# Performance work log

Measured on AMD Instinct MI355X. Metric: run time of the kernel, lower is better.

The kernel has to match this reference:

```python
import jax, jax.numpy as jnp
import numpy as np

EPS = 2.220446049250313e-16  # sys.float_info.epsilon, as in repo's feature_normalize
H_BW = 0.1  # bandwidth h (forward default)


def _feature_normalize(f):
    # L2 normalize over channel dim (dim=1) of [B, C, H, W]
    norm = jnp.sqrt(jnp.sum(f * f, axis=1, keepdims=True)) + EPS
    return f / norm


def setup_inputs() -> dict:
    key = jax.random.key(0)
    k1, k2 = jax.random.split(key)
    shape = (4, 256, 64, 64)
    return {
        "X_features": jax.random.normal(k1, shape, dtype=jnp.float32),
        "Y_features": jax.random.normal(k2, shape, dtype=jnp.float32),
    }


def reference(X_features, Y_features):
    B, C = X_features.shape[0], X_features.shape[1]
    # feature centering (opt.PONO = False branch): subtract Y's per-channel spatial mean
    y_mean = jnp.mean(Y_features.reshape(B, C, -1), axis=-1)[:, :, None, None]
    Xc = X_features - y_mean
    Yc = Y_features - y_mean
    # channel-wise L2 normalize, then flatten spatial dims -> [B, C, N]
    Xn = _feature_normalize(Xc).reshape(B, C, -1)
    Yn = _feature_normalize(Yc).reshape(B, C, -1)
    # pairwise cosine distance d: [B, N, N]
    d = 1.0 - jnp.einsum("bcn,bcm->bnm", Xn, Yn)
    # relative distance normalization by row-min
    d_min = jnp.min(d, axis=-1, keepdims=True)
    d_norm = d / (d_min + 0.001)
    # softmax-like contextual similarity weights
    w = jnp.exp((1.0 - d_norm) / H_BW)
    A_ij = w / jnp.sum(w, axis=-1, keepdims=True)
    # per-sample contextual similarity and loss
    CX = jnp.mean(jnp.max(A_ij, axis=-1), axis=1)  # [B]
    loss = -jnp.log(CX)
    return loss
```

## Files before the change

kernel.cpp:

```cpp
#include <hip/hip_runtime.h>
#include <hip/hip_bf16.h>
#include <stdint.h>


#define Bn 4
#define Cn 256
#define Nn 4096

typedef float  f32x16 __attribute__((ext_vector_type(16)));
typedef __bf16 bf16x8 __attribute__((ext_vector_type(8)));

#define GLD16(gp, lp) __builtin_amdgcn_global_load_lds(                      \
    (const __attribute__((address_space(1))) void*)(gp),                     \
    (__attribute__((address_space(3))) void*)(lp), 16, 0, 0)

#define LDbf(base, off) (*(const bf16x8*)((base) + (off)))
#define MFMA32(a, b, c) __builtin_amdgcn_mfma_f32_32x32x16_bf16((a), (b), (c), 0, 0, 0)

__global__ __launch_bounds__(256) void k_mean(const float* __restrict__ Y,
                                              float* __restrict__ ymean) {
  const int bc = blockIdx.x;
  const float4* p4 = (const float4*)(Y + (size_t)bc * 4096);
  float s = 0.f;
  #pragma unroll
  for (int i = 0; i < 4; ++i) {
    float4 v = p4[threadIdx.x + i * 256];
    s += (v.x + v.y) + (v.z + v.w);
  }
  #pragma unroll
  for (int m = 1; m < 64; m <<= 1) s += __shfl_xor(s, m);
  __shared__ float part[4];
  if ((threadIdx.x & 63) == 0) part[threadIdx.x >> 6] = s;
  __syncthreads();
  if (threadIdx.x == 0)
    ymean[bc] = (part[0] + part[1] + part[2] + part[3]) * (1.0f / 4096.0f);
}

__global__ __launch_bounds__(256) void k_pack(const float* __restrict__ X,
                                              const float* __restrict__ Y,
                                              const float* __restrict__ ymean,
                                              __hip_bfloat16* __restrict__ Xp,
                                              __hip_bfloat16* __restrict__ Yp,
                                              float* __restrict__ invnx,
                                              float* __restrict__ invny) {
  const int n0 = blockIdx.x * 64, b = blockIdx.y;
  __shared__ float mu[256];
  __shared__ float tile[64][65];
  __shared__ float part[8][64];
  const int t  = threadIdx.x;
  const int tc = t >> 6, tn = t & 63;
  const int oc = t & 63, on = t >> 6;
  mu[t] = ymean[b * 256 + t];
  __syncthreads();
  float psx = 0.f, psy = 0.f;
  for (int cc = 0; cc < 4; ++cc) {
    #pragma unroll 4
    for (int i = 0; i < 16; ++i) {
      int cl = i * 4 + tc;
      float v = X[((size_t)b * 256 + cc * 64 + cl) * 4096 + n0 + tn] - mu[cc * 64 + cl];
      tile[cl][tn] = v;
      psx += v * v;
    }
    __syncthreads();
    #pragma unroll 4
    for (int i = 0; i < 16; ++i) {
      int nl = i * 4 + on;
      Xp[((size_t)b * 4096 + n0 + nl) * 256 + cc * 64 + oc] = __float2bfloat16(tile[oc][nl]);
    }
    __syncthreads();
    #pragma unroll 4
    for (int i = 0; i < 16; ++i) {
      int cl = i * 4 + tc;
      float v = Y[((size_t)b * 256 + cc * 64 + cl) * 4096 + n0 + tn] - mu[cc * 64 + cl];
      tile[cl][tn] = v;
      psy += v * v;
    }
    __syncthreads();
    #pragma unroll 4
    for (int i = 0; i < 16; ++i) {
      int nl = i * 4 + on;
      Yp[((size_t)b * 4096 + n0 + nl) * 256 + cc * 64 + oc] = __float2bfloat16(tile[oc][nl]);
    }
    __syncthreads();
  }
  part[tc][tn] = psx;
  part[4 + tc][tn] = psy;
  __syncthreads();
  if (t < 64)
    invnx[b * 4096 + n0 + t] = rsqrtf(part[0][t] + part[1][t] + part[2][t] + part[3][t]);
  else if (t < 128) {
    int u = t - 64;
    invny[b * 4096 + n0 + u] = rsqrtf(part[4][u] + part[5][u] + part[6][u] + part[7][u]);
  }
}

template<int PASS>
__global__ __launch_bounds__(512, 1) void k_pass(const __hip_bfloat16* __restrict__ Xp,
                                                 const __hip_bfloat16* __restrict__ Yp,
                                                 const float* __restrict__ invnx,
                                                 const float* __restrict__ invny,
                                                 float* __restrict__ rmax_part,
                                                 float* __restrict__ ssum_part) {
  __shared__ __align__(16) char YsL[3][32768];
  __shared__ float invnyL[2048];
  __shared__ float redm[2][2][2][16][4];
  __shared__ float2 lammuL[128];

  const int tid = threadIdx.x;
  const int lane = tid & 63;
  const int w = tid >> 6;
  const int rg = w >> 2, cs = w & 3;
  const int l31 = lane & 31, hi = lane >> 5;
  const int hi16 = hi << 4;

  const int L = blockIdx.x;
  const int b = (L & 7) >> 1, half = L & 1;
  const int rowtile = L >> 3;
  const int rowg0 = b * Nn + rowtile * 128;
  const int colg0 = half * 2048;

  const char* Xgb = (const char*)Xp + (size_t)rowg0 * 512;
  const char* Yg  = (const char*)(Yp + ((size_t)b * Nn + colg0) * Cn);

  bf16x8 A[4][4][2];
  #pragma unroll
  for (int kp = 0; kp < 4; ++kp)
    #pragma unroll
    for (int s = 0; s < 4; ++s)
      #pragma unroll
      for (int ai = 0; ai < 2; ++ai)
        A[kp][s][ai] = *(const bf16x8*)(Xgb + (size_t)(rg * 64 + ai * 32 + l31) * 512
                                            + ((kp * 4 + s) * 32 + hi16));

  ((float4*)invnyL)[tid] = ((const float4*)(invny + b * Nn + colg0))[tid];
  if constexpr (PASS == 2) {
    if (tid < 128) {
      int rowg = rowg0 + tid;
      float mg = fmaxf(rmax_part[rowg], rmax_part[Bn * Nn + rowg]);
      float ix = invnx[rowg];
      float smax = mg * ix;
      float lam = (10.0f / (1.001f - smax)) * ix * 1.44269504f;
      lammuL[tid] = make_float2(lam, lam * mg);
    }
  }
  __syncthreads();

  int yoff[4];
  #pragma unroll
  for (int i = 0; i < 4; ++i) {
    int m = i * 64 + (tid >> 3);
    yoff[i] = m * 512 + (((tid & 7) * 16) ^ ((m & 7) << 4));
  }

#define STAGE_HALF(q, h)                                                      \
  { const int q_ = (q);                                                       \
    const char* src_ = Yg + (size_t)((q_ >> 2) * 131072 + (q_ & 3) * 128);    \
    char* dst_ = YsL[q_ % 3];                                                 \
    GLD16(src_ + yoff[2 * (h)],     dst_ + (2 * (h)) * 8192 + tid * 16);      \
    GLD16(src_ + yoff[2 * (h) + 1], dst_ + (2 * (h) + 1) * 8192 + tid * 16); }

  STAGE_HALF(0, 0); STAGE_HALF(0, 1);
  STAGE_HALF(1, 0); STAGE_HALF(1, 1);

  const int brow0 = cs * 64 + l31;
  const int bswz  = (brow0 & 7) << 4;

  f32x16 acc[2][2];
  #pragma unroll
  for (int ai = 0; ai < 2; ++ai)
    #pragma unroll
    for (int bj = 0; bj < 2; ++bj) acc[ai][bj] = (f32x16)0.0f;
  float accR[2][16];
  #pragma unroll
  for (int ai = 0; ai < 2; ++ai)
    #pragma unroll
    for (int r = 0; r < 16; ++r) accR[ai][r] = (PASS == 1) ? -3.0e38f : 0.f;

#define HARVEST()                                                             \
  { const int cb = mt * 256 + cs * 64 + l31;                                  \
    const float iny0 = invnyL[cb], iny1 = invnyL[cb + 32];                    \
    _Pragma("unroll")                                                         \
    for (int ai = 0; ai < 2; ++ai) {                                          \
      _Pragma("unroll")                                                       \
      for (int r = 0; r < 16; ++r) {                                          \
        if constexpr (PASS == 1) {                                            \
          accR[ai][r] = fmaxf(accR[ai][r],                                    \
              fmaxf(acc[ai][0][r] * iny0, acc[ai][1][r] * iny1));             \
        } else {                                                              \
          float2 lm = lammuL[rg * 64 + ai * 32 + (r & 3) + 8 * (r >> 2) + 4 * hi]; \
          accR[ai][r] += exp2f(fmaf(lm.x, acc[ai][0][r] * iny0, -lm.y))       \
                       + exp2f(fmaf(lm.x, acc[ai][1][r] * iny1, -lm.y));      \
        }                                                                     \
        acc[ai][0][r] = 0.f; acc[ai][1][r] = 0.f;                             \
      } } }

#define QUAD(KP, S, KB)                                                       \
  { bf16x8 b0_ = LDbf(yb_, brow0 * 128 + (((KB) + hi16) ^ bswz));             \
    bf16x8 b1_ = LDbf(yb_, (brow0 + 32) * 128 + (((KB) + hi16) ^ bswz));      \
    __builtin_amdgcn_s_setprio(1);                                            \
    acc[0][0] = MFMA32(A[KP][S][0], b0_, acc[0][0]);                          \
    acc[0][1] = MFMA32(A[KP][S][0], b1_, acc[0][1]);                          \
    acc[1][0] = MFMA32(A[KP][S][1], b0_, acc[1][0]);                          \
    acc[1][1] = MFMA32(A[KP][S][1], b1_, acc[1][1]);                          \
    __builtin_amdgcn_s_setprio(0); }

#define TILE(KP, WAITS, DO_STAGE)                                             \
  { const int p_ = mt * 4 + (KP);                                             \
    if (DO_STAGE) STAGE_HALF(p_ + 2, 0);                                      \
    asm volatile("s_waitcnt vmcnt(" WAITS ")" ::: "memory");                  \
    asm volatile("s_barrier" ::: "memory");                                   \
    const char* yb_ = YsL[p_ % 3];                                            \
    QUAD(KP, 0, 0)                                                            \
    QUAD(KP, 1, 32)                                                           \
    if (DO_STAGE) STAGE_HALF(p_ + 2, 1);                                      \
    QUAD(KP, 2, 64)                                                           \
    QUAD(KP, 3, 96)                                                           \
    if ((KP) == 3) HARVEST();                                                 \
    asm volatile("s_barrier" ::: "memory"); }

  for (int mt = 0; mt < 7; ++mt) {
    TILE(0, "6", true)
    TILE(1, "6", true)
    TILE(2, "6", true)
    TILE(3, "6", true)
  }
  {
    const int mt = 7;
    TILE(0, "6", true)
    TILE(1, "6", true)
    TILE(2, "4", false)
    TILE(3, "0", false)
  }
#undef TILE
#undef QUAD
#undef HARVEST
#undef STAGE_HALF

  #pragma unroll
  for (int ai = 0; ai < 2; ++ai)
    #pragma unroll
    for (int r = 0; r < 16; ++r) {
      float v = accR[ai][r];
      #pragma unroll
      for (int m = 1; m < 32; m <<= 1) {
        float o = __shfl_xor(v, m);
        v = (PASS == 1) ? fmaxf(v, o) : (v + o);
      }
      if (l31 == 0) redm[rg][hi][ai][r][cs] = v;
    }
  __syncthreads();
  if (tid < 128) {
    const int rgg = tid >> 6, rr = tid & 63;
    const int aii = (rr >> 5) & 1, r32 = rr & 31;
    const int hh = (r32 >> 2) & 1;
    const int reg = (r32 & 3) | (((r32 >> 3) & 3) << 2);
    float v0 = redm[rgg][hh][aii][reg][0], v1 = redm[rgg][hh][aii][reg][1];
    float v2 = redm[rgg][hh][aii][reg][2], v3 = redm[rgg][hh][aii][reg][3];
    if constexpr (PASS == 1)
      rmax_part[half * (Bn * Nn) + rowg0 + tid] = fmaxf(fmaxf(v0, v1), fmaxf(v2, v3));
    else
      ssum_part[half * (Bn * Nn) + rowg0 + tid] = v0 + v1 + v2 + v3;
  }
}

__global__ __launch_bounds__(256) void k_fin(const float* __restrict__ ssum_part,
                                             float* __restrict__ out) {
  const int b = blockIdx.x;
  float s = 0.f;
  #pragma unroll 4
  for (int i = 0; i < 16; ++i) {
    int row = b * Nn + threadIdx.x + i * 256;
    s += 1.0f / (ssum_part[row] + ssum_part[Bn * Nn + row]);
  }
  #pragma unroll
  for (int m = 1; m < 64; m <<= 1) s += __shfl_xor(s, m);
  __shared__ float part[4];
  if ((threadIdx.x & 63) == 0) part[threadIdx.x >> 6] = s;
  __syncthreads();
  if (threadIdx.x == 0)
    out[b] = -logf((part[0] + part[1] + part[2] + part[3]) * (1.0f / (float)Nn));
}

extern "C" void kernel_launch(void* const* d_in, const int* in_sizes, int n_in,
                              void* d_out, int out_size, void* d_ws, size_t ws_size,
                              hipStream_t stream) {
  const float* X = (const float*)d_in[0];
  const float* Y = (const float*)d_in[1];
  float* out = (float*)d_out;
  char* ws = (char*)d_ws;

  __hip_bfloat16* Xp = (__hip_bfloat16*)ws;
  __hip_bfloat16* Yp = (__hip_bfloat16*)(ws + 8388608);
  float* invnx = (float*)(ws + 16777216);
  float* invny = invnx + 16384;
  float* rmax  = invny + 16384;
  float* ssum  = rmax + 32768;
  float* ymean = ssum + 32768;

  k_mean  <<<Bn * Cn, 256, 0, stream>>>(Y, ymean);
  k_pack  <<<dim3(Nn / 64, Bn), 256, 0, stream>>>(X, Y, ymean, Xp, Yp, invnx, invny);
  k_pass<1><<<256, 512, 0, stream>>>(Xp, Yp, invnx, invny, rmax, ssum);
  k_pass<2><<<256, 512, 0, stream>>>(Xp, Yp, invnx, invny, rmax, ssum);
  k_fin   <<<Bn, 256, 0, stream>>>(ssum, out);
}
```

Baseline: 228.9 us.

## Move upper half of X operand from registers to swizzled LDS

Keeps only the first two K-slices of the X (A) operand in registers and stages the other half into a new 32 KB swizzled LDS buffer with async global-to-LDS loads. Tiles 2 and 3 of each column block now read A fragments from LDS alongside the B fragments. The kernel attribute changes from one block per CU to a 2-waves-per-EU hint, with the aim of cutting VGPR pressure and allowing more resident waves. In exchange it doubles LDS read traffic in half of the tiles and raises LDS use to roughly 137 KB, which likely still limits the CU to one 512-thread block.

```diff
diff --git a/kernel.cpp b/kernel.cpp
--- a/kernel.cpp
+++ b/kernel.cpp
@@ -95,13 +95,16 @@
 }
 
 template<int PASS>
-__global__ __launch_bounds__(512, 1) void k_pass(const __hip_bfloat16* __restrict__ Xp,
-                                                 const __hip_bfloat16* __restrict__ Yp,
-                                                 const float* __restrict__ invnx,
-                                                 const float* __restrict__ invny,
-                                                 float* __restrict__ rmax_part,
-                                                 float* __restrict__ ssum_part) {
+__global__ __launch_bounds__(512)
+__attribute__((amdgpu_waves_per_eu(2, 2)))
+void k_pass(const __hip_bfloat16* __restrict__ Xp,
+            const __hip_bfloat16* __restrict__ Yp,
+            const float* __restrict__ invnx,
+            const float* __restrict__ invny,
+            float* __restrict__ rmax_part,
+            float* __restrict__ ssum_part) {
   __shared__ __align__(16) char YsL[3][32768];
+  __shared__ __align__(16) char AsL[32768];
   __shared__ float invnyL[2048];
   __shared__ float redm[2][2][2][16][4];
   __shared__ float2 lammuL[128];
@@ -122,9 +125,9 @@
   const char* Xgb = (const char*)Xp + (size_t)rowg0 * 512;
   const char* Yg  = (const char*)(Yp + ((size_t)b * Nn + colg0) * Cn);
 
-  bf16x8 A[4][4][2];
-  #pragma unroll
-  for (int kp = 0; kp < 4; ++kp)
+  bf16x8 A[2][4][2];
+  #pragma unroll
+  for (int kp = 0; kp < 2; ++kp)
     #pragma unroll
     for (int s = 0; s < 4; ++s)
       #pragma unroll
@@ -145,6 +148,14 @@
   }
   __syncthreads();
 
+  #pragma unroll
+  for (int s = 0; s < 4; ++s) {
+    const int off = s * 8192 + tid * 16;
+    const int row = off >> 8;
+    const int col = off & 255;
+    GLD16(Xgb + (size_t)row * 512 + 256 + (col ^ ((row & 7) << 4)), AsL + off);
+  }
+
   int yoff[4];
   #pragma unroll
   for (int i = 0; i < 4; ++i) {
@@ -164,6 +175,8 @@
 
   const int brow0 = cs * 64 + l31;
   const int bswz  = (brow0 & 7) << 4;
+  const int arow0 = rg * 64 + l31;
+  const int aswz  = (l31 & 7) << 4;
 
   f32x16 acc[2][2];
   #pragma unroll
@@ -194,7 +207,7 @@
         acc[ai][0][r] = 0.f; acc[ai][1][r] = 0.f;                             \
       } } }
 
-#define QUAD(KP, S, KB)                                                       \
+#define QUAD_R(KP, S, KB)                                                     \
   { bf16x8 b0_ = LDbf(yb_, brow0 * 128 + (((KB) + hi16) ^ bswz));             \
     bf16x8 b1_ = LDbf(yb_, (brow0 + 32) * 128 + (((KB) + hi16) ^ bswz));      \
     __builtin_amdgcn_s_setprio(1);                                            \
@@ -204,35 +217,63 @@
     acc[1][1] = MFMA32(A[KP][S][1], b1_, acc[1][1]);                          \
     __builtin_amdgcn_s_setprio(0); }
 
-#define TILE(KP, WAITS, DO_STAGE)                                             \
-  { const int p_ = mt * 4 + (KP);                                             \
+#define QUAD_L(KP, S, KB)                                                     \
+  { const int ka_ = (((KP) - 2) * 4 + (S)) * 32 + hi16;                       \
+    bf16x8 a0_ = LDbf(AsL, arow0 * 256 + (ka_ ^ aswz));                       \
+    bf16x8 a1_ = LDbf(AsL, (arow0 + 32) * 256 + (ka_ ^ aswz));                \
+    bf16x8 b0_ = LDbf(yb_, brow0 * 128 + (((KB) + hi16) ^ bswz));             \
+    bf16x8 b1_ = LDbf(yb_, (brow0 + 32) * 128 + (((KB) + hi16) ^ bswz));      \
+    __builtin_amdgcn_s_setprio(1);                                            \
+    acc[0][0] = MFMA32(a0_, b0_, acc[0][0]);                                  \
+    acc[0][1] = MFMA32(a0_, b1_, acc[0][1]);                                  \
+    acc[1][0] = MFMA32(a1_, b0_, acc[1][0]);                                  \
+    acc[1][1] = MFMA32(a1_, b1_, acc[1][1]);                                  \
+    __builtin_amdgcn_s_setprio(0); }
+
+#define TILE_HEAD(KP, WAITS, DO_STAGE)                                        \
+    const int p_ = mt * 4 + (KP);                                             \
     if (DO_STAGE) STAGE_HALF(p_ + 2, 0);                                      \
     asm volatile("s_waitcnt vmcnt(" WAITS ")" ::: "memory");                  \
     asm volatile("s_barrier" ::: "memory");                                   \
-    const char* yb_ = YsL[p_ % 3];                                            \
-    QUAD(KP, 0, 0)                                                            \
-    QUAD(KP, 1, 32)                                                           \
+    const char* yb_ = YsL[p_ % 3];
+
+#define TILE_R(KP, WAITS, DO_STAGE)                                           \
+  { TILE_HEAD(KP, WAITS, DO_STAGE)                                            \
+    QUAD_R(KP, 0, 0)                                                          \
+    QUAD_R(KP, 1, 32)                                                         \
     if (DO_STAGE) STAGE_HALF(p_ + 2, 1);                                      \
-    QUAD(KP, 2, 64)                                                           \
-    QUAD(KP, 3, 96)                                                           \
+    QUAD_R(KP, 2, 64)                                                         \
+    QUAD_R(KP, 3, 96)                                                         \
+    asm volatile("s_barrier" ::: "memory"); }
+
+#define TILE_L(KP, WAITS, DO_STAGE)                                           \
+  { TILE_HEAD(KP, WAITS, DO_STAGE)                                            \
+    QUAD_L(KP, 0, 0)                                                          \
+    QUAD_L(KP, 1, 32)                                                         \
+    if (DO_STAGE) STAGE_HALF(p_ + 2, 1);                                      \
+    QUAD_L(KP, 2, 64)                                                         \
+    QUAD_L(KP, 3, 96)                                                         \
     if ((KP) == 3) HARVEST();                                                 \
     asm volatile("s_barrier" ::: "memory"); }
 
   for (int mt = 0; mt < 7; ++mt) {
-    TILE(0, "6", true)
-    TILE(1, "6", true)
-    TILE(2, "6", true)
-    TILE(3, "6", true)
+    TILE_R(0, "6", true)
+    TILE_R(1, "6", true)
+    TILE_L(2, "6", true)
+    TILE_L(3, "6", true)
   }
   {
     const int mt = 7;
-    TILE(0, "6", true)
-    TILE(1, "6", true)
-    TILE(2, "4", false)
-    TILE(3, "0", false)
-  }
-#undef TILE
-#undef QUAD
+    TILE_R(0, "6", true)
+    TILE_R(1, "6", true)
+    TILE_L(2, "4", false)
+    TILE_L(3, "0", false)
+  }
+#undef TILE_R
+#undef TILE_L
+#undef TILE_HEAD
+#undef QUAD_R
+#undef QUAD_L
 #undef HARVEST
 #undef STAGE_HALF
 
```

Result: faster. 200.6 us (-12.4%).

## Restructure Y staging into 4-slot ring with double-K super-tiles

Applied to the files above, without the earlier changes.

Replaces the 3-buffer half-tile staging pipeline with a 4-slot LDS ring. Each iteration stages two full K-tiles and runs 16 MFMAs per barrier pair, which halves the number of barriers and vmcnt waits per column tile. It also loads four B fragments at once before each group of eight MFMAs. LDS use grows by 32 KB per block, and the launch attribute changes from launch_bounds(512,1) to waves_per_eu(2,2), which can change the register budget. The deeper prefetch and fewer syncs are meant to hide global-load latency, at the risk of register pressure or reduced occupancy.

```diff
diff --git a/kernel.cpp b/kernel.cpp
--- a/kernel.cpp
+++ b/kernel.cpp
@@ -95,13 +95,15 @@
 }
 
 template<int PASS>
-__global__ __launch_bounds__(512, 1) void k_pass(const __hip_bfloat16* __restrict__ Xp,
-                                                 const __hip_bfloat16* __restrict__ Yp,
-                                                 const float* __restrict__ invnx,
-                                                 const float* __restrict__ invny,
-                                                 float* __restrict__ rmax_part,
-                                                 float* __restrict__ ssum_part) {
-  __shared__ __align__(16) char YsL[3][32768];
+__global__ __launch_bounds__(512)
+__attribute__((amdgpu_waves_per_eu(2, 2)))
+void k_pass(const __hip_bfloat16* __restrict__ Xp,
+            const __hip_bfloat16* __restrict__ Yp,
+            const float* __restrict__ invnx,
+            const float* __restrict__ invny,
+            float* __restrict__ rmax_part,
+            float* __restrict__ ssum_part) {
+  __shared__ __align__(16) char YsL[4][32768];
   __shared__ float invnyL[2048];
   __shared__ float redm[2][2][2][16][4];
   __shared__ float2 lammuL[128];
@@ -152,15 +154,16 @@
     yoff[i] = m * 512 + (((tid & 7) * 16) ^ ((m & 7) << 4));
   }
 
-#define STAGE_HALF(q, h)                                                      \
+#define STAGE_FULL(q)                                                         \
   { const int q_ = (q);                                                       \
     const char* src_ = Yg + (size_t)((q_ >> 2) * 131072 + (q_ & 3) * 128);    \
-    char* dst_ = YsL[q_ % 3];                                                 \
-    GLD16(src_ + yoff[2 * (h)],     dst_ + (2 * (h)) * 8192 + tid * 16);      \
-    GLD16(src_ + yoff[2 * (h) + 1], dst_ + (2 * (h) + 1) * 8192 + tid * 16); }
-
-  STAGE_HALF(0, 0); STAGE_HALF(0, 1);
-  STAGE_HALF(1, 0); STAGE_HALF(1, 1);
+    char* dst_ = YsL[q_ & 3];                                                 \
+    GLD16(src_ + yoff[0], dst_ + 0 * 8192 + tid * 16);                        \
+    GLD16(src_ + yoff[1], dst_ + 1 * 8192 + tid * 16);                        \
+    GLD16(src_ + yoff[2], dst_ + 2 * 8192 + tid * 16);                        \
+    GLD16(src_ + yoff[3], dst_ + 3 * 8192 + tid * 16); }
+
+  STAGE_FULL(0); STAGE_FULL(1);
 
   const int brow0 = cs * 64 + l31;
   const int bswz  = (brow0 & 7) << 4;
@@ -194,47 +197,50 @@
         acc[ai][0][r] = 0.f; acc[ai][1][r] = 0.f;                             \
       } } }
 
-#define QUAD(KP, S, KB)                                                       \
-  { bf16x8 b0_ = LDbf(yb_, brow0 * 128 + (((KB) + hi16) ^ bswz));             \
-    bf16x8 b1_ = LDbf(yb_, (brow0 + 32) * 128 + (((KB) + hi16) ^ bswz));      \
+#define OCT(YB, KP, S0)                                                       \
+  { bf16x8 b00 = LDbf(YB, brow0 * 128 + ((((S0) * 32) + hi16) ^ bswz));       \
+    bf16x8 b01 = LDbf(YB, (brow0 + 32) * 128 + ((((S0) * 32) + hi16) ^ bswz));\
+    bf16x8 b10 = LDbf(YB, brow0 * 128 + ((((S0) * 32 + 32) + hi16) ^ bswz));  \
+    bf16x8 b11 = LDbf(YB, (brow0 + 32) * 128 + ((((S0) * 32 + 32) + hi16) ^ bswz)); \
     __builtin_amdgcn_s_setprio(1);                                            \
-    acc[0][0] = MFMA32(A[KP][S][0], b0_, acc[0][0]);                          \
-    acc[0][1] = MFMA32(A[KP][S][0], b1_, acc[0][1]);                          \
-    acc[1][0] = MFMA32(A[KP][S][1], b0_, acc[1][0]);                          \
-    acc[1][1] = MFMA32(A[KP][S][1], b1_, acc[1][1]);                          \
+    acc[0][0] = MFMA32(A[KP][S0][0], b00, acc[0][0]);                         \
+    acc[0][1] = MFMA32(A[KP][S0][0], b01, acc[0][1]);                         \
+    acc[1][0] = MFMA32(A[KP][S0][1], b00, acc[1][0]);                         \
+    acc[1][1] = MFMA32(A[KP][S0][1], b01, acc[1][1]);                         \
+    acc[0][0] = MFMA32(A[KP][S0 + 1][0], b10, acc[0][0]);                     \
+    acc[0][1] = MFMA32(A[KP][S0 + 1][0], b11, acc[0][1]);                     \
+    acc[1][0] = MFMA32(A[KP][S0 + 1][1], b10, acc[1][0]);                     \
+    acc[1][1] = MFMA32(A[KP][S0 + 1][1], b11, acc[1][1]);                     \
     __builtin_amdgcn_s_setprio(0); }
 
-#define TILE(KP, WAITS, DO_STAGE)                                             \
-  { const int p_ = mt * 4 + (KP);                                             \
-    if (DO_STAGE) STAGE_HALF(p_ + 2, 0);                                      \
+#define STILE(HK, WAITS, DO_STAGE)                                            \
+  { const int P_ = mt * 2 + (HK);                                             \
+    if (DO_STAGE) STAGE_FULL(2 * P_ + 2);                                     \
     asm volatile("s_waitcnt vmcnt(" WAITS ")" ::: "memory");                  \
     asm volatile("s_barrier" ::: "memory");                                   \
-    const char* yb_ = YsL[p_ % 3];                                            \
-    QUAD(KP, 0, 0)                                                            \
-    QUAD(KP, 1, 32)                                                           \
-    if (DO_STAGE) STAGE_HALF(p_ + 2, 1);                                      \
-    QUAD(KP, 2, 64)                                                           \
-    QUAD(KP, 3, 96)                                                           \
-    if ((KP) == 3) HARVEST();                                                 \
+    const char* yb0_ = YsL[(2 * P_) & 3];                                     \
+    const char* yb1_ = YsL[(2 * P_ + 1) & 3];                                 \
+    OCT(yb0_, 2 * (HK), 0)                                                    \
+    if (DO_STAGE) STAGE_FULL(2 * P_ + 3);                                     \
+    OCT(yb0_, 2 * (HK), 2)                                                    \
+    OCT(yb1_, 2 * (HK) + 1, 0)                                                \
+    OCT(yb1_, 2 * (HK) + 1, 2)                                                \
+    if ((HK) == 1) HARVEST();                                                 \
     asm volatile("s_barrier" ::: "memory"); }
 
   for (int mt = 0; mt < 7; ++mt) {
-    TILE(0, "6", true)
-    TILE(1, "6", true)
-    TILE(2, "6", true)
-    TILE(3, "6", true)
+    STILE(0, "4", true)
+    STILE(1, "4", true)
   }
   {
     const int mt = 7;
-    TILE(0, "6", true)
-    TILE(1, "6", true)
-    TILE(2, "4", false)
-    TILE(3, "0", false)
-  }
-#undef TILE
-#undef QUAD
+    STILE(0, "4", true)
+    STILE(1, "0", false)
+  }
+#undef STILE
+#undef OCT
 #undef HARVEST
-#undef STAGE_HALF
+#undef STAGE_FULL
 
   #pragma unroll
   for (int ai = 0; ai < 2; ++ai)
```

Measured after the change: 220.8 us. -3.5%, faster.
